# Optimization experiments

Hardware: AMD Instinct MI355X
Metric: run time of the kernel (lower is better)

## Reference

```python
import jax, jax.numpy as jnp
import numpy as np

EMBED_DIM = 1024
NUM_HEADS = 16
HEAD_DIM = EMBED_DIM // NUM_HEADS
SCALING = HEAD_DIM ** (-0.5)
LN_EPS = 1e-5


def setup_inputs() -> dict:
    key = jax.random.key(0)
    ks = jax.random.split(key, 6)
    N, L, D = 2, 2048, EMBED_DIM
    x = jax.random.normal(ks[0], (N, L, D), dtype=jnp.float32)
    W_in = jax.random.normal(ks[1], (3 * D, D), dtype=jnp.float32) * 0.02
    b_in = jnp.zeros((3 * D,), dtype=jnp.float32)
    Wc = jax.random.normal(ks[2], (HEAD_DIM, HEAD_DIM), dtype=jnp.float32) * 0.1
    bc = jnp.zeros((HEAD_DIM,), dtype=jnp.float32)
    ln_gamma = jnp.ones((HEAD_DIM,), dtype=jnp.float32)
    ln_beta = jnp.zeros((HEAD_DIM,), dtype=jnp.float32)
    W_out = jax.random.normal(ks[3], (D, D), dtype=jnp.float32) * 0.02
    b_out = jnp.zeros((D,), dtype=jnp.float32)
    return {"x": x, "W_in": W_in, "b_in": b_in, "Wc": Wc, "bc": bc,
            "ln_gamma": ln_gamma, "ln_beta": ln_beta, "W_out": W_out, "b_out": b_out}


def _reshape_heads(t, N, L):
    # (N, L, D) -> (N*H, L, head_dim)
    return t.reshape(N, L, NUM_HEADS, HEAD_DIM).transpose(0, 2, 1, 3).reshape(N * NUM_HEADS, L, HEAD_DIM)


def reference(x, W_in, b_in, Wc, bc, ln_gamma, ln_beta, W_out, b_out):
    N, L, D = x.shape
    qkv = jnp.einsum('nld,ed->nle', x, W_in) + b_in  # (N, L, 3D)
    q, k, v = jnp.split(qkv, 3, axis=-1)
    q_head = _reshape_heads(q, N, L)  # (B, L, HD) with B = N*H
    k_head = _reshape_heads(k, N, L)
    v_head = _reshape_heads(v, N, L)

    # Conv1d with kernel_size=1 == pointwise linear on head_dim channels
    q_temp = jnp.einsum('blc,oc->blo', q_head, Wc) + bc
    q_temp = jax.nn.gelu(q_temp, approximate=False)  # torch nn.GELU() is exact erf
    mu = q_temp.mean(axis=-1, keepdims=True)
    var = q_temp.var(axis=-1, keepdims=True)
    q_temp = (q_temp - mu) / jnp.sqrt(var + LN_EPS) * ln_gamma + ln_beta

    q_rel = q_temp.mean(axis=1)  # (B, HD) -- mean over sequence
    # one kernel row per (batch, head): (B, L)
    W_kernel_row = jnp.einsum('bd,bld->bl', q_rel * SCALING, k_head)

    # Toeplitz attention matrix: attn[b, i, j] = W_kernel_row[b, |i-j|]
    idx = jnp.arange(L)
    lags = jnp.abs(idx[:, None] - idx[None, :])  # (L, L), already in [0, L-1]
    attn = W_kernel_row[:, lags]  # (B, L, L) gather

    causal_mask = lags * jnp.sign(idx[None, :] - idx[:, None]) > 0  # j > i
    causal_mask = jnp.triu(jnp.ones((L, L), dtype=bool), k=1)
    attn = jnp.where(causal_mask[None, :, :], -jnp.inf, attn)
    weights = jax.nn.softmax(attn, axis=-1)  # (B, L, L); dropout=0 -> identity

    attn_out = jnp.einsum('bij,bjd->bid', weights, v_head)  # (B, L, HD)
    attn_out = attn_out.reshape(N, NUM_HEADS, L, HEAD_DIM).transpose(0, 2, 1, 3).reshape(N, L, D)
    output = jnp.einsum('nld,ed->nle', attn_out, W_out) + b_out
    return output, weights.mean(axis=1)
```

## Files before the change

kernel.cpp:

```cpp
#include <hip/hip_runtime.h>
#include <math.h>

#define L_SEQ 2048
#define D_EMB 1024
#define NHEADS 16
#define HD 64
#define BHEADS 32
#define NBATCH 2
#define LN_EPS 1e-5f
#define SCALING 0.125f

typedef __attribute__((ext_vector_type(8))) __bf16 bf16x8;
typedef __attribute__((ext_vector_type(4))) float f32x4;
typedef const __attribute__((address_space(1))) unsigned int* gptr_as1;
typedef __attribute__((address_space(3))) unsigned int* lptr_as3;

__device__ __forceinline__ void load16_to_lds(const void* g, void* l) {
  __builtin_amdgcn_global_load_lds((gptr_as1)g, (lptr_as3)l, 16, 0, 0);
}

__device__ __forceinline__ unsigned short f2bf(float f) {
  unsigned int u = __float_as_uint(f);
  u += 0x7fff + ((u >> 16) & 1);
  return (unsigned short)(u >> 16);
}

__device__ __forceinline__ float bflo(unsigned int u) { return __uint_as_float(u << 16); }
__device__ __forceinline__ float bfhi(unsigned int u) { return __uint_as_float(u & 0xffff0000u); }
__device__ __forceinline__ float bf2f(unsigned short us) {
  return __uint_as_float((unsigned int)us << 16);
}

__global__ __launch_bounds__(256) void cvt4_bf16_kernel(
    const float* __restrict__ a, int na, const float* __restrict__ b, int nb,
    const float* __restrict__ c, int nc, const float* __restrict__ d, int nd,
    unsigned short* __restrict__ oa, unsigned short* __restrict__ ob,
    unsigned short* __restrict__ oc, unsigned short* __restrict__ od) {
  int i = (blockIdx.x * 256 + threadIdx.x) * 4;
  const float* src;
  unsigned short* dst;
  int j;
  if (i < na) { src = a; dst = oa; j = i; }
  else if (i < na + nb) { src = b; dst = ob; j = i - na; }
  else if (i < na + nb + nc) { src = c; dst = oc; j = i - na - nb; }
  else if (i < na + nb + nc + nd) { src = d; dst = od; j = i - na - nb - nc; }
  else return;
  float4 v = *(const float4*)&src[j];
  ushort4 o;
  o.x = f2bf(v.x); o.y = f2bf(v.y); o.z = f2bf(v.z); o.w = f2bf(v.w);
  *(ushort4*)&dst[j] = o;
}

__global__ __launch_bounds__(256) void gemm_qv(
    const unsigned short* __restrict__ A, const unsigned short* __restrict__ B,
    const float* __restrict__ bias, unsigned short* __restrict__ qbf,
    unsigned short* __restrict__ vT, int K) {
  __shared__ unsigned short As[4096];
  __shared__ unsigned short Bs[4096];
  const int id = blockIdx.y * 16 + blockIdx.x;
  const int by = (id >> 5) * 2 + (id & 1);
  const int bx = (id & 31) >> 1;
  const int bm = by * 128;
  const int bn = bx * 128;
  const int woff = (bn < D_EMB) ? 0 : D_EMB;
  const int tid = threadIdx.x;
  const int lane = tid & 63;
  const int wave = tid >> 6;
  const int wr = (wave >> 1) * 64;
  const int wc = (wave & 1) * 64;

  const int c0 = tid, c1 = tid + 256;
  const unsigned short* ga0 = A + (size_t)(bm + (c0 >> 6) * 16 + (c0 & 15)) * K + ((c0 >> 4) & 3) * 8;
  const unsigned short* ga1 = A + (size_t)(bm + (c1 >> 6) * 16 + (c1 & 15)) * K + ((c1 >> 4) & 3) * 8;
  const unsigned short* gb0 = B + (size_t)(bn + woff + (c0 >> 6) * 16 + (c0 & 15)) * K + ((c0 >> 4) & 3) * 8;
  const unsigned short* gb1 = B + (size_t)(bn + woff + (c1 >> 6) * 16 + (c1 & 15)) * K + ((c1 >> 4) & 3) * 8;

  f32x4 acc[4][4] = {};
  for (int k0 = 0; k0 < K; k0 += 32) {
    load16_to_lds(ga0 + k0, &As[c0 * 8]);
    load16_to_lds(ga1 + k0, &As[c1 * 8]);
    load16_to_lds(gb0 + k0, &Bs[c0 * 8]);
    load16_to_lds(gb1 + k0, &Bs[c1 * 8]);
    __syncthreads();
    bf16x8 af[4], bf[4];
    #pragma unroll
    for (int i = 0; i < 4; ++i)
      af[i] = *(const bf16x8*)&As[((wr >> 4) + i) * 512 + lane * 8];
    #pragma unroll
    for (int j = 0; j < 4; ++j)
      bf[j] = *(const bf16x8*)&Bs[((wc >> 4) + j) * 512 + lane * 8];
    #pragma unroll
    for (int i = 0; i < 4; ++i)
      #pragma unroll
      for (int j = 0; j < 4; ++j)
        acc[i][j] = __builtin_amdgcn_mfma_f32_16x16x32_bf16(af[i], bf[j], acc[i][j], 0, 0, 0);
    __syncthreads();
  }
  const int lc = lane & 15;
  const int lr4 = (lane >> 4) << 2;
  float bv[4];
  #pragma unroll
  for (int j = 0; j < 4; ++j) bv[j] = bias[bn + woff + wc + j * 16 + lc];
  if (bn < D_EMB) {
    #pragma unroll
    for (int i = 0; i < 4; ++i)
      #pragma unroll
      for (int r = 0; r < 4; ++r) {
        const int row = bm + wr + i * 16 + lr4 + r;
        unsigned short* cp = &qbf[(size_t)row * D_EMB + bn + wc + lc];
        #pragma unroll
        for (int j = 0; j < 4; ++j) cp[j * 16] = f2bf(acc[i][j][r] + bv[j]);
      }
  } else {
    #pragma unroll
    for (int i = 0; i < 4; ++i) {
      const int row0 = bm + wr + i * 16 + lr4;
      const int n = row0 >> 11;
      const int jseq = row0 & (L_SEQ - 1);
      #pragma unroll
      for (int j = 0; j < 4; ++j) {
        const int cv = (bn - D_EMB) + wc + j * 16 + lc;
        const int d = cv & 63;
        const int h = cv >> 6;
        ushort4 o;
        o.x = f2bf(acc[i][j][0] + bv[j]);
        o.y = f2bf(acc[i][j][1] + bv[j]);
        o.z = f2bf(acc[i][j][2] + bv[j]);
        o.w = f2bf(acc[i][j][3] + bv[j]);
        *(ushort4*)&vT[(size_t)((n * 16 + h) * 64 + d) * L_SEQ + jseq] = o;
      }
    }
  }
}

__global__ __launch_bounds__(256) void gemm_out64(
    const unsigned short* __restrict__ A, const unsigned short* __restrict__ B,
    const float* __restrict__ bias, float* __restrict__ C,
    int M, int Nn, int K) {
  __shared__ unsigned short As[2048];
  __shared__ unsigned short Bs[4096];
  const int bm = blockIdx.y * 64;
  const int bn = blockIdx.x * 128;
  const int tid = threadIdx.x;
  const int lane = tid & 63;
  const int wave = tid >> 6;
  const int wr = (wave >> 1) * 32;
  const int wc = (wave & 1) * 64;

  const int ca = tid;
  const int cb0 = tid, cb1 = tid + 256;
  const unsigned short* ga = A + (size_t)(bm + (ca >> 6) * 16 + (ca & 15)) * K + ((ca >> 4) & 3) * 8;
  const unsigned short* gb0 = B + (size_t)(bn + (cb0 >> 6) * 16 + (cb0 & 15)) * K + ((cb0 >> 4) & 3) * 8;
  const unsigned short* gb1 = B + (size_t)(bn + (cb1 >> 6) * 16 + (cb1 & 15)) * K + ((cb1 >> 4) & 3) * 8;

  f32x4 acc[2][4] = {};
  for (int k0 = 0; k0 < K; k0 += 32) {
    load16_to_lds(ga + k0, &As[ca * 8]);
    load16_to_lds(gb0 + k0, &Bs[cb0 * 8]);
    load16_to_lds(gb1 + k0, &Bs[cb1 * 8]);
    __syncthreads();
    bf16x8 af[2], bf[4];
    #pragma unroll
    for (int i = 0; i < 2; ++i)
      af[i] = *(const bf16x8*)&As[((wr >> 4) + i) * 512 + lane * 8];
    #pragma unroll
    for (int j = 0; j < 4; ++j)
      bf[j] = *(const bf16x8*)&Bs[((wc >> 4) + j) * 512 + lane * 8];
    #pragma unroll
    for (int i = 0; i < 2; ++i)
      #pragma unroll
      for (int j = 0; j < 4; ++j)
        acc[i][j] = __builtin_amdgcn_mfma_f32_16x16x32_bf16(af[i], bf[j], acc[i][j], 0, 0, 0);
    __syncthreads();
  }
  const int lc = lane & 15;
  const int lr4 = (lane >> 4) << 2;
  float bv[4];
  #pragma unroll
  for (int j = 0; j < 4; ++j) bv[j] = bias[bn + wc + j * 16 + lc];
  #pragma unroll
  for (int i = 0; i < 2; ++i)
    #pragma unroll
    for (int r = 0; r < 4; ++r) {
      const int row = bm + wr + i * 16 + lr4 + r;
      float* cp = &C[(size_t)row * Nn + bn + wc + lc];
      #pragma unroll
      for (int j = 0; j < 4; ++j) cp[j * 16] = acc[i][j][r] + bv[j];
    }
}

__global__ __launch_bounds__(256) void qtemp_mfma_kernel(
    const unsigned short* __restrict__ q_bf, const unsigned short* __restrict__ Wc_bf,
    const float* __restrict__ bc, const float* __restrict__ gamma,
    const float* __restrict__ beta, float* __restrict__ q_rel_part) {
  __shared__ unsigned short Qs[8192];
  __shared__ unsigned short Ws[4096];
  __shared__ float red[4][64];
  const int b = blockIdx.y;
  const int n = b >> 4, h = b & 15;
  const int l0 = blockIdx.x * 128;
  const int tid = threadIdx.x;
  const int lane = tid & 63;
  const int wave = tid >> 6;
  const int quad = lane >> 4;
  const int mi = lane & 15;

  #pragma unroll
  for (int s = 0; s < 4; ++s) {
    const int c = tid + s * 256;
    const int row = ((c >> 7) << 4) + (c & 15);
    const int kof = ((c >> 4) & 7) << 3;
    load16_to_lds(q_bf + (size_t)(n * L_SEQ + l0 + row) * D_EMB + h * 64 + kof,
                  &Qs[c * 8]);
  }
  #pragma unroll
  for (int s = 0; s < 2; ++s) {
    const int c = tid + s * 256;
    const int row = ((c >> 7) << 4) + (c & 15);
    const int kof = ((c >> 4) & 7) << 3;
    load16_to_lds(Wc_bf + row * 64 + kof, &Ws[c * 8]);
  }
  __syncthreads();

  f32x4 acc[2][4] = {};
  #pragma unroll
  for (int kk = 0; kk < 2; ++kk) {
    const int fo = ((kk * 4 + quad) * 16 + mi) * 8;
    bf16x8 bf[4];
    #pragma unroll
    for (int t = 0; t < 4; ++t) bf[t] = *(const bf16x8*)&Ws[t * 1024 + fo];
    #pragma unroll
    for (int isub = 0; isub < 2; ++isub) {
      const bf16x8 af = *(const bf16x8*)&Qs[(wave * 2 + isub) * 1024 + fo];
      #pragma unroll
      for (int t = 0; t < 4; ++t)
        acc[isub][t] = __builtin_amdgcn_mfma_f32_16x16x32_bf16(af, bf[t], acc[isub][t], 0, 0, 0);
    }
  }

  float bcv[4], gav[4], bev[4], colacc[4];
  #pragma unroll
  for (int t = 0; t < 4; ++t) {
    const int col = t * 16 + mi;
    bcv[t] = bc[col]; gav[t] = gamma[col]; bev[t] = beta[col];
    colacc[t] = 0.f;
  }
  #pragma unroll
  for (int isub = 0; isub < 2; ++isub) {
    #pragma unroll
    for (int r = 0; r < 4; ++r) {
      float g[4];
      float s1 = 0.f, s2 = 0.f;
      #pragma unroll
      for (int t = 0; t < 4; ++t) {
        const float d = acc[isub][t][r] + bcv[t];
        const float gg = 0.5f * d * (1.f + erff(d * 0.70710678118654752f));
        g[t] = gg;
        s1 += gg;
        s2 += gg * gg;
      }
      #pragma unroll
      for (int off = 8; off > 0; off >>= 1) {
        s1 += __shfl_xor(s1, off);
        s2 += __shfl_xor(s2, off);
      }
      const float mu = s1 * (1.f / 64.f);
      const float var = s2 * (1.f / 64.f) - mu * mu;
      const float rs = rsqrtf(var + LN_EPS);
      #pragma unroll
      for (int t = 0; t < 4; ++t)
        colacc[t] += (g[t] - mu) * rs * gav[t] + bev[t];
    }
  }
  #pragma unroll
  for (int t = 0; t < 4; ++t) {
    colacc[t] += __shfl_xor(colacc[t], 16);
    colacc[t] += __shfl_xor(colacc[t], 32);
  }
  if (quad == 0) {
    #pragma unroll
    for (int t = 0; t < 4; ++t) red[wave][t * 16 + mi] = colacc[t];
  }
  __syncthreads();
  if (wave == 0) {
    float tot = red[0][lane] + red[1][lane] + red[2][lane] + red[3][lane];
    q_rel_part[((size_t)b * 16 + blockIdx.x) * 64 + lane] = tot;
  }
}

__global__ __launch_bounds__(256) void zw_kernel(
    const float* __restrict__ part, const unsigned short* __restrict__ Win_bf,
    const float* __restrict__ b_in, const unsigned short* __restrict__ x_bf,
    float* __restrict__ w_row) {
  const int b = blockIdx.x;
  const int n = b >> 4, h = b & 15;
  const int tid = threadIdx.x;
  __shared__ float qrel[64];
  __shared__ float zsh[1024];
  __shared__ float ts[64];
  __shared__ float kbs;
  if (tid < 64) {
    float s = 0.f;
    #pragma unroll
    for (int c = 0; c < 16; ++c) s += part[((size_t)b * 16 + c) * 64 + tid];
    qrel[tid] = s;
    ts[tid] = s * b_in[D_EMB + h * 64 + tid];
  }
  __syncthreads();
  if (tid == 0) {
    float kb = 0.f;
    #pragma unroll
    for (int d = 0; d < 64; ++d) kb += ts[d];
    kbs = kb * (SCALING / (float)L_SEQ);
  }
  {
    const int j0 = tid * 4;
    float4 z4 = make_float4(0.f, 0.f, 0.f, 0.f);
    const unsigned short* wp = Win_bf + (size_t)(D_EMB + h * 64) * D_EMB + j0;
    #pragma unroll 4
    for (int d = 0; d < 64; ++d) {
      ushort4 w4 = *(const ushort4*)(wp + (size_t)d * D_EMB);
      const float qd = qrel[d];
      z4.x += qd * bf2f(w4.x);
      z4.y += qd * bf2f(w4.y);
      z4.z += qd * bf2f(w4.z);
      z4.w += qd * bf2f(w4.w);
    }
    const float sc = SCALING / (float)L_SEQ;
    zsh[j0 + 0] = z4.x * sc;
    zsh[j0 + 1] = z4.y * sc;
    zsh[j0 + 2] = z4.z * sc;
    zsh[j0 + 3] = z4.w * sc;
  }
  __syncthreads();
  const int t = blockIdx.y * 256 + tid;
  const unsigned short* xr = x_bf + (size_t)(n * L_SEQ + t) * D_EMB;
  float acc = kbs;
  #pragma unroll 4
  for (int c = 0; c < D_EMB; c += 8) {
    float4 zl = *(const float4*)&zsh[c];
    float4 zh = *(const float4*)&zsh[c + 4];
    uint4 xv = *(const uint4*)&xr[c];
    acc += zl.x * bflo(xv.x) + zl.y * bfhi(xv.x)
         + zl.z * bflo(xv.y) + zl.w * bfhi(xv.y)
         + zh.x * bflo(xv.z) + zh.y * bfhi(xv.z)
         + zh.z * bflo(xv.w) + zh.w * bfhi(xv.w);
  }
  w_row[b * L_SEQ + t] = acc;
}

__global__ __launch_bounds__(256) void scan_kernel(
    const float* __restrict__ w_row, float* __restrict__ e_out,
    float* __restrict__ inv_out) {
  const int b = blockIdx.x;
  const int tid = threadIdx.x;
  __shared__ float sh[L_SEQ];
  __shared__ float ts[256];
  const float* wb = w_row + b * L_SEQ;
  float m = -3.4e38f;
  for (int i = tid; i < L_SEQ; i += 256) {
    float v = wb[i];
    sh[i] = v;
    m = fmaxf(m, v);
  }
  ts[tid] = m;
  __syncthreads();
  for (int off = 128; off > 0; off >>= 1) {
    if (tid < off) ts[tid] = fmaxf(ts[tid], ts[tid + off]);
    __syncthreads();
  }
  const float mx = ts[0];
  __syncthreads();
  const int t0 = tid * 8;
  float loc[8];
  float run = 0.f;
  #pragma unroll
  for (int k = 0; k < 8; ++k) {
    float ev = expf(sh[t0 + k] - mx);
    e_out[b * L_SEQ + t0 + k] = ev;
    run += ev;
    loc[k] = run;
  }
  ts[tid] = run;
  __syncthreads();
  for (int off = 1; off < 256; off <<= 1) {
    float v = ts[tid];
    float add = (tid >= off) ? ts[tid - off] : 0.f;
    __syncthreads();
    ts[tid] = v + add;
    __syncthreads();
  }
  float prefix = (tid > 0) ? ts[tid - 1] : 0.f;
  #pragma unroll
  for (int k = 0; k < 8; ++k)
    inv_out[b * L_SEQ + t0 + k] = 1.f / (prefix + loc[k]);
}

__global__ __launch_bounds__(256) void conv_mfma_kernel(
    const unsigned short* __restrict__ vT, const float* __restrict__ e_arr,
    const float* __restrict__ inv_arr, unsigned short* __restrict__ attn_out) {
  __shared__ unsigned short V_s[2][2048];
  __shared__ unsigned short rep[2][8 * 320];
  const int blk = 7 - blockIdx.x;
  const int b = blockIdx.y;
  const int dh = blockIdx.z;
  const int n = b >> 4, h = b & 15;
  const int blkI = blk * 256;
  const int blk4 = blk * 4;
  const int njt = blk4 + 4;
  const int tid = threadIdx.x;
  const int lane = tid & 63;
  const int wave = tid >> 6;
  const int quad = lane >> 4;
  const int mi = lane & 15;
  const float* e_b = e_arr + b * L_SEQ;

  const unsigned short* vsrc = vT +
      (size_t)(b * 64 + dh * 32 + (tid >> 7) * 16 + (tid & 15)) * L_SEQ + ((tid >> 4) & 7) * 8;

  f32x4 acc[4][2] = {};

  {
    load16_to_lds(vsrc, &V_s[0][tid * 8]);
    const int lagBase = blkI;
    int v = tid;
    int lag = lagBase + 256 - v;
    float ev = (lag >= 0 && lag < L_SEQ) ? e_b[lag] : 0.f;
    unsigned short bfv = f2bf(ev);
    #pragma unroll
    for (int r = 0; r < 8; ++r) { int idx = v - r; if (idx >= 0) rep[0][r * 320 + idx] = bfv; }
    if (tid < 64) {
      v = tid + 256;
      lag = lagBase - tid;
      ev = (lag >= 0 && lag < L_SEQ) ? e_b[lag] : 0.f;
      bfv = f2bf(ev);
      #pragma unroll
      for (int r = 0; r < 8; ++r) rep[0][r * 320 + (v - r)] = bfv;
    }
  }

  for (int jt = 0; jt < njt; ++jt) {
    __syncthreads();
    const int cb = jt & 1;
    if (jt + 1 < njt) {
      const int pb = cb ^ 1;
      const int j0 = (jt + 1) * 64;
      load16_to_lds(vsrc + j0, &V_s[pb][tid * 8]);
      const int lagBase = blkI - j0;
      int v = tid;
      int lag = lagBase + 256 - v;
      float ev = (lag >= 0 && lag < L_SEQ) ? e_b[lag] : 0.f;
      unsigned short bfv = f2bf(ev);
      #pragma unroll
      for (int r = 0; r < 8; ++r) { int idx = v - r; if (idx >= 0) rep[pb][r * 320 + idx] = bfv; }
      if (tid < 64) {
        v = tid + 256;
        lag = lagBase - tid;
        ev = (lag >= 0 && lag < L_SEQ) ? e_b[lag] : 0.f;
        bfv = f2bf(ev);
        #pragma unroll
        for (int r = 0; r < 8; ++r) rep[pb][r * 320 + (v - r)] = bfv;
      }
    }
    if (jt <= blk4 + wave) {
      const unsigned short* Vb = V_s[cb];
      const unsigned short* Rb = rep[cb];
      bf16x8 ef[6];
      #pragma unroll
      for (int q = 0; q < 6; ++q) {
        const int s = 256 - wave * 64 - mi + quad * 8 - 16 * (q - 2);
        const int rr = s & 7;
        ef[q] = *(const bf16x8*)&Rb[rr * 320 + (s - rr)];
      }
      #pragma unroll
      for (int kk = 0; kk < 2; ++kk) {
        bf16x8 bv[2];
        #pragma unroll
        for (int t = 0; t < 2; ++t)
          bv[t] = *(const bf16x8*)&Vb[t * 1024 + kk * 512 + lane * 8];
        #pragma unroll
        for (int isub = 0; isub < 4; ++isub) {
          const int qi = isub - 2 * kk + 2;
          #pragma unroll
          for (int t = 0; t < 2; ++t)
            acc[isub][t] = __builtin_amdgcn_mfma_f32_16x16x32_bf16(ef[qi], bv[t], acc[isub][t], 0, 0, 0);
        }
      }
    }
  }
  #pragma unroll
  for (int isub = 0; isub < 4; ++isub) {
    #pragma unroll
    for (int r = 0; r < 4; ++r) {
      const int i = blkI + wave * 64 + isub * 16 + quad * 4 + r;
      const float iv = inv_arr[b * L_SEQ + i];
      unsigned short* op = &attn_out[((size_t)(n * L_SEQ + i)) * D_EMB + h * 64 + dh * 32 + mi];
      #pragma unroll
      for (int t = 0; t < 2; ++t) op[t * 16] = f2bf(acc[isub][t][r] * iv);
    }
  }
}

__global__ __launch_bounds__(256) void wmean_kernel(
    const float* __restrict__ e_arr, const float* __restrict__ inv_arr,
    float* __restrict__ out_wm) {
  const int b = blockIdx.x;
  __shared__ float e_s[L_SEQ];
  __shared__ float inv_s[L_SEQ];
  __shared__ float red[256];
  const int tid = threadIdx.x;
  for (int i = tid; i < L_SEQ; i += 256) {
    e_s[i] = e_arr[b * L_SEQ + i];
    inv_s[i] = inv_arr[b * L_SEQ + i];
  }
  __syncthreads();
  const int jj = tid & 127;
  const int h2 = tid >> 7;
  const int j = blockIdx.y * 128 + jj;
  float acc = 0.f;
  for (int d = h2; j + d < L_SEQ; d += 2) acc += e_s[d] * inv_s[j + d];
  red[tid] = acc;
  __syncthreads();
  if (tid < 128)
    out_wm[b * L_SEQ + j] = (red[tid] + red[tid + 128]) * (1.f / (float)L_SEQ);
}

extern "C" void kernel_launch(void* const* d_in, const int* in_sizes, int n_in,
                              void* d_out, int out_size, void* d_ws, size_t ws_size,
                              hipStream_t stream) {
  const float* x       = (const float*)d_in[0];
  const float* W_in    = (const float*)d_in[1];
  const float* b_in    = (const float*)d_in[2];
  const float* Wc      = (const float*)d_in[3];
  const float* bc      = (const float*)d_in[4];
  const float* gamma   = (const float*)d_in[5];
  const float* beta    = (const float*)d_in[6];
  const float* W_out   = (const float*)d_in[7];
  const float* b_out   = (const float*)d_in[8];
  float* out = (float*)d_out;

  const int M = NBATCH * L_SEQ;
  char* ws = (char*)d_ws;
  unsigned short* xa_bf  = (unsigned short*)ws;
  unsigned short* Win_bf = (unsigned short*)(ws + 8388608);
  unsigned short* Wout_bf= (unsigned short*)(ws + 14680064);
  unsigned short* Wc_bf  = (unsigned short*)(ws + 16777216);
  unsigned short* q_bf   = (unsigned short*)(ws + 16785408);
  unsigned short* vT     = (unsigned short*)(ws + 25174016);
  float* part  = (float*)(ws + 33562624);
  float* w_row = (float*)(ws + 33693696);
  float* e_arr = (float*)(ws + 33955840);
  float* inv_a = (float*)(ws + 34217984);

  {
    const int na = M * D_EMB, nb = 3 * D_EMB * D_EMB, nc = D_EMB * D_EMB, nd = HD * HD;
    cvt4_bf16_kernel<<<dim3((na + nb + nc + nd) / 1024), 256, 0, stream>>>(
        x, na, W_in, nb, W_out, nc, Wc, nd, xa_bf, Win_bf, Wout_bf, Wc_bf);
  }
  gemm_qv<<<dim3(16, 32), 256, 0, stream>>>(xa_bf, Win_bf, b_in, q_bf, vT, D_EMB);
  qtemp_mfma_kernel<<<dim3(16, BHEADS), 256, 0, stream>>>(
      q_bf, Wc_bf, bc, gamma, beta, part);
  zw_kernel<<<dim3(BHEADS, 8), 256, 0, stream>>>(part, Win_bf, b_in, xa_bf, w_row);
  scan_kernel<<<dim3(BHEADS), 256, 0, stream>>>(w_row, e_arr, inv_a);
  wmean_kernel<<<dim3(BHEADS, L_SEQ / 128), 256, 0, stream>>>(
      e_arr, inv_a, out + (size_t)M * D_EMB);
  conv_mfma_kernel<<<dim3(8, BHEADS, 2), 256, 0, stream>>>(vT, e_arr, inv_a, xa_bf);
  gemm_out64<<<dim3(D_EMB / 128, M / 64), 256, 0, stream>>>(
      xa_bf, Wout_bf, b_out, out, M, D_EMB, D_EMB);
}
```

Measured before the change: 283.7 us.

## Precompute shifted bf16 Toeplitz kernel rows in scan, enlarge conv tiles

The scan kernel now also writes eight shifted, reversed bf16 copies of the exp row to global memory. The Toeplitz MFMA conv kernel can then read its A fragments directly from that buffer instead of rebuilding replicated LDS tiles every iteration. The conv loop now works on 256-wide V tiles with four async loads per thread, and it drops the per-wave causal skip, so the last tile is partly computed on zeros. wmean is launched with twice as many blocks and a 4-way split, and the extra workspace buffer adds a small amount of global traffic.

```diff
diff --git a/kernel.cpp b/kernel.cpp
--- a/kernel.cpp
+++ b/kernel.cpp
@@ -9,6 +9,7 @@
 #define NBATCH 2
 #define LN_EPS 1e-5f
 #define SCALING 0.125f
+#define EREP_STRIDE 2304
 
 typedef __attribute__((ext_vector_type(8))) __bf16 bf16x8;
 typedef __attribute__((ext_vector_type(4))) float f32x4;
@@ -351,7 +352,7 @@
 
 __global__ __launch_bounds__(256) void scan_kernel(
     const float* __restrict__ w_row, float* __restrict__ e_out,
-    float* __restrict__ inv_out) {
+    float* __restrict__ inv_out, unsigned short* __restrict__ erep) {
   const int b = blockIdx.x;
   const int tid = threadIdx.x;
   __shared__ float sh[L_SEQ];
@@ -378,6 +379,7 @@
   for (int k = 0; k < 8; ++k) {
     float ev = expf(sh[t0 + k] - mx);
     e_out[b * L_SEQ + t0 + k] = ev;
+    sh[t0 + k] = ev;
     run += ev;
     loc[k] = run;
   }
@@ -394,109 +396,94 @@
   #pragma unroll
   for (int k = 0; k < 8; ++k)
     inv_out[b * L_SEQ + t0 + k] = 1.f / (prefix + loc[k]);
+  for (int idx = tid; idx < 8 * (EREP_STRIDE / 4); idx += 256) {
+    const int r = idx / (EREP_STRIDE / 4);
+    const int x4 = (idx - r * (EREP_STRIDE / 4)) * 4;
+    const int src = 2047 - x4 - r;
+    ushort4 o;
+    o.x = (src >= 0)     ? f2bf(sh[src])     : (unsigned short)0;
+    o.y = (src - 1 >= 0) ? f2bf(sh[src - 1]) : (unsigned short)0;
+    o.z = (src - 2 >= 0) ? f2bf(sh[src - 2]) : (unsigned short)0;
+    o.w = (src - 3 >= 0) ? f2bf(sh[src - 3]) : (unsigned short)0;
+    *(ushort4*)&erep[((size_t)b * 8 + r) * EREP_STRIDE + x4] = o;
+  }
 }
 
 __global__ __launch_bounds__(256) void conv_mfma_kernel(
-    const unsigned short* __restrict__ vT, const float* __restrict__ e_arr,
+    const unsigned short* __restrict__ vT, const unsigned short* __restrict__ erep,
     const float* __restrict__ inv_arr, unsigned short* __restrict__ attn_out) {
-  __shared__ unsigned short V_s[2][2048];
-  __shared__ unsigned short rep[2][8 * 320];
+  __shared__ unsigned short V_s[2][8192];
   const int blk = 7 - blockIdx.x;
   const int b = blockIdx.y;
   const int dh = blockIdx.z;
   const int n = b >> 4, h = b & 15;
   const int blkI = blk * 256;
-  const int blk4 = blk * 4;
-  const int njt = blk4 + 4;
+  const int ntiles = blk + 1;
   const int tid = threadIdx.x;
   const int lane = tid & 63;
   const int wave = tid >> 6;
   const int quad = lane >> 4;
   const int mi = lane & 15;
-  const float* e_b = e_arr + b * L_SEQ;
-
-  const unsigned short* vsrc = vT +
-      (size_t)(b * 64 + dh * 32 + (tid >> 7) * 16 + (tid & 15)) * L_SEQ + ((tid >> 4) & 7) * 8;
+
+  const unsigned short* vsrc[4];
+  #pragma unroll
+  for (int s = 0; s < 4; ++s) {
+    const int c = tid + s * 256;
+    vsrc[s] = vT + (size_t)(b * 64 + dh * 32 + (c >> 9) * 16 + (c & 15)) * L_SEQ + ((c >> 4) & 31) * 8;
+  }
+
+  const int r = (2047 - mi) & 7;
+  const unsigned short* eb = erep + ((size_t)b * 8 + r) * EREP_STRIDE;
+  const int ub0 = 2047 - blkI - wave * 64 - mi + quad * 8 - r;
 
   f32x4 acc[4][2] = {};
 
-  {
-    load16_to_lds(vsrc, &V_s[0][tid * 8]);
-    const int lagBase = blkI;
-    int v = tid;
-    int lag = lagBase + 256 - v;
-    float ev = (lag >= 0 && lag < L_SEQ) ? e_b[lag] : 0.f;
-    unsigned short bfv = f2bf(ev);
-    #pragma unroll
-    for (int r = 0; r < 8; ++r) { int idx = v - r; if (idx >= 0) rep[0][r * 320 + idx] = bfv; }
-    if (tid < 64) {
-      v = tid + 256;
-      lag = lagBase - tid;
-      ev = (lag >= 0 && lag < L_SEQ) ? e_b[lag] : 0.f;
-      bfv = f2bf(ev);
-      #pragma unroll
-      for (int r = 0; r < 8; ++r) rep[0][r * 320 + (v - r)] = bfv;
-    }
-  }
-
-  for (int jt = 0; jt < njt; ++jt) {
+  #pragma unroll
+  for (int s = 0; s < 4; ++s) load16_to_lds(vsrc[s], &V_s[0][(tid + s * 256) * 8]);
+
+  for (int jt = 0; jt < ntiles; ++jt) {
     __syncthreads();
     const int cb = jt & 1;
-    if (jt + 1 < njt) {
-      const int pb = cb ^ 1;
-      const int j0 = (jt + 1) * 64;
-      load16_to_lds(vsrc + j0, &V_s[pb][tid * 8]);
-      const int lagBase = blkI - j0;
-      int v = tid;
-      int lag = lagBase + 256 - v;
-      float ev = (lag >= 0 && lag < L_SEQ) ? e_b[lag] : 0.f;
-      unsigned short bfv = f2bf(ev);
-      #pragma unroll
-      for (int r = 0; r < 8; ++r) { int idx = v - r; if (idx >= 0) rep[pb][r * 320 + idx] = bfv; }
-      if (tid < 64) {
-        v = tid + 256;
-        lag = lagBase - tid;
-        ev = (lag >= 0 && lag < L_SEQ) ? e_b[lag] : 0.f;
-        bfv = f2bf(ev);
-        #pragma unroll
-        for (int r = 0; r < 8; ++r) rep[pb][r * 320 + (v - r)] = bfv;
+    if (jt + 1 < ntiles) {
+      #pragma unroll
+      for (int s = 0; s < 4; ++s)
+        load16_to_lds(vsrc[s] + (jt + 1) * 256, &V_s[cb ^ 1][(tid + s * 256) * 8]);
+    }
+    const unsigned short* Vb = V_s[cb];
+    const int ub = ub0 + jt * 256;
+    bf16x8 f0 = *(const bf16x8*)&eb[ub];
+    bf16x8 f1 = *(const bf16x8*)&eb[ub - 16];
+    bf16x8 f2 = *(const bf16x8*)&eb[ub - 32];
+    bf16x8 f3 = *(const bf16x8*)&eb[ub - 48];
+    #pragma unroll
+    for (int kk = 0; kk < 8; ++kk) {
+      const bf16x8 b0 = *(const bf16x8*)&Vb[(((kk * 4 + quad) * 16 + mi)) * 8];
+      const bf16x8 b1 = *(const bf16x8*)&Vb[((512 + (kk * 4 + quad) * 16 + mi)) * 8];
+      acc[0][0] = __builtin_amdgcn_mfma_f32_16x16x32_bf16(f0, b0, acc[0][0], 0, 0, 0);
+      acc[0][1] = __builtin_amdgcn_mfma_f32_16x16x32_bf16(f0, b1, acc[0][1], 0, 0, 0);
+      acc[1][0] = __builtin_amdgcn_mfma_f32_16x16x32_bf16(f1, b0, acc[1][0], 0, 0, 0);
+      acc[1][1] = __builtin_amdgcn_mfma_f32_16x16x32_bf16(f1, b1, acc[1][1], 0, 0, 0);
+      acc[2][0] = __builtin_amdgcn_mfma_f32_16x16x32_bf16(f2, b0, acc[2][0], 0, 0, 0);
+      acc[2][1] = __builtin_amdgcn_mfma_f32_16x16x32_bf16(f2, b1, acc[2][1], 0, 0, 0);
+      acc[3][0] = __builtin_amdgcn_mfma_f32_16x16x32_bf16(f3, b0, acc[3][0], 0, 0, 0);
+      acc[3][1] = __builtin_amdgcn_mfma_f32_16x16x32_bf16(f3, b1, acc[3][1], 0, 0, 0);
+      f2 = f0;
+      f3 = f1;
+      if (kk < 7) {
+        f0 = *(const bf16x8*)&eb[ub + 32 * (kk + 1)];
+        f1 = *(const bf16x8*)&eb[ub + 32 * kk + 16];
       }
     }
-    if (jt <= blk4 + wave) {
-      const unsigned short* Vb = V_s[cb];
-      const unsigned short* Rb = rep[cb];
-      bf16x8 ef[6];
-      #pragma unroll
-      for (int q = 0; q < 6; ++q) {
-        const int s = 256 - wave * 64 - mi + quad * 8 - 16 * (q - 2);
-        const int rr = s & 7;
-        ef[q] = *(const bf16x8*)&Rb[rr * 320 + (s - rr)];
-      }
-      #pragma unroll
-      for (int kk = 0; kk < 2; ++kk) {
-        bf16x8 bv[2];
-        #pragma unroll
-        for (int t = 0; t < 2; ++t)
-          bv[t] = *(const bf16x8*)&Vb[t * 1024 + kk * 512 + lane * 8];
-        #pragma unroll
-        for (int isub = 0; isub < 4; ++isub) {
-          const int qi = isub - 2 * kk + 2;
-          #pragma unroll
-          for (int t = 0; t < 2; ++t)
-            acc[isub][t] = __builtin_amdgcn_mfma_f32_16x16x32_bf16(ef[qi], bv[t], acc[isub][t], 0, 0, 0);
-        }
-      }
-    }
   }
   #pragma unroll
   for (int isub = 0; isub < 4; ++isub) {
     #pragma unroll
-    for (int r = 0; r < 4; ++r) {
-      const int i = blkI + wave * 64 + isub * 16 + quad * 4 + r;
+    for (int rr = 0; rr < 4; ++rr) {
+      const int i = blkI + wave * 64 + isub * 16 + quad * 4 + rr;
       const float iv = inv_arr[b * L_SEQ + i];
       unsigned short* op = &attn_out[((size_t)(n * L_SEQ + i)) * D_EMB + h * 64 + dh * 32 + mi];
       #pragma unroll
-      for (int t = 0; t < 2; ++t) op[t * 16] = f2bf(acc[isub][t][r] * iv);
+      for (int t = 0; t < 2; ++t) op[t * 16] = f2bf(acc[isub][t][rr] * iv);
     }
   }
 }
@@ -514,15 +501,16 @@
     inv_s[i] = inv_arr[b * L_SEQ + i];
   }
   __syncthreads();
-  const int jj = tid & 127;
-  const int h2 = tid >> 7;
-  const int j = blockIdx.y * 128 + jj;
+  const int jj = tid & 63;
+  const int ds = tid >> 6;
+  const int j = blockIdx.y * 64 + jj;
   float acc = 0.f;
-  for (int d = h2; j + d < L_SEQ; d += 2) acc += e_s[d] * inv_s[j + d];
+  for (int d = ds; j + d < L_SEQ; d += 4) acc += e_s[d] * inv_s[j + d];
   red[tid] = acc;
   __syncthreads();
-  if (tid < 128)
-    out_wm[b * L_SEQ + j] = (red[tid] + red[tid + 128]) * (1.f / (float)L_SEQ);
+  if (tid < 64)
+    out_wm[b * L_SEQ + j] =
+        (red[jj] + red[jj + 64] + red[jj + 128] + red[jj + 192]) * (1.f / (float)L_SEQ);
 }
 
 extern "C" void kernel_launch(void* const* d_in, const int* in_sizes, int n_in,
@@ -551,6 +539,7 @@
   float* w_row = (float*)(ws + 33693696);
   float* e_arr = (float*)(ws + 33955840);
   float* inv_a = (float*)(ws + 34217984);
+  unsigned short* erep   = (unsigned short*)(ws + 34480128);
 
   {
     const int na = M * D_EMB, nb = 3 * D_EMB * D_EMB, nc = D_EMB * D_EMB, nd = HD * HD;
@@ -561,10 +550,10 @@
   qtemp_mfma_kernel<<<dim3(16, BHEADS), 256, 0, stream>>>(
       q_bf, Wc_bf, bc, gamma, beta, part);
   zw_kernel<<<dim3(BHEADS, 8), 256, 0, stream>>>(part, Win_bf, b_in, xa_bf, w_row);
-  scan_kernel<<<dim3(BHEADS), 256, 0, stream>>>(w_row, e_arr, inv_a);
-  wmean_kernel<<<dim3(BHEADS, L_SEQ / 128), 256, 0, stream>>>(
+  scan_kernel<<<dim3(BHEADS), 256, 0, stream>>>(w_row, e_arr, inv_a, erep);
+  wmean_kernel<<<dim3(BHEADS, L_SEQ / 64), 256, 0, stream>>>(
       e_arr, inv_a, out + (size_t)M * D_EMB);
-  conv_mfma_kernel<<<dim3(8, BHEADS, 2), 256, 0, stream>>>(vT, e_arr, inv_a, xa_bf);
+  conv_mfma_kernel<<<dim3(8, BHEADS, 2), 256, 0, stream>>>(vT, erep, inv_a, xa_bf);
   gemm_out64<<<dim3(D_EMB / 128, M / 64), 256, 0, stream>>>(
       xa_bf, Wout_bf, b_out, out, M, D_EMB, D_EMB);
 }
```

New measurement: 268.0 us. 5.5% less time.
